# Performance work log

Measured on AMD Instinct MI355X. Metric: run time of the kernel, lower is better.

The kernel has to match this reference:

```python
import jax, jax.numpy as jnp
import numpy as np

TOK, CPC, RHY = 135, 12, 8
HID, STACK, KEY, EMB = 400, 32, 300, 50
B, T = 1, 4096


def setup_inputs() -> dict:
    key = jax.random.key(0)
    ks = jax.random.split(key, 32)
    w = lambda k, shape, s=0.05: jax.random.normal(k, shape, jnp.float32) * s
    inp = {
        'xr': jax.random.randint(ks[0], (B, T), 0, RHY, dtype=jnp.int32),
        'xcpc': jax.random.randint(ks[1], (B, T), 0, CPC, dtype=jnp.int32),
        'xma': jax.random.randint(ks[2], (B, T), 0, TOK, dtype=jnp.int32),
        'emb_midi': w(ks[3], (TOK, EMB)),
        'emb_cpc': w(ks[4], (CPC, EMB)),
        'emb_rhythm': w(ks[5], (RHY, EMB)),
        # note_rnn: 2-layer LSTM, input 3*EMB=150, hidden 400 (torch gate order i,f,g,o)
        'note_Wih0': w(ks[6], (4 * HID, 3 * EMB)),
        'note_Whh0': w(ks[7], (4 * HID, HID)),
        'note_bih0': w(ks[8], (4 * HID,)),
        'note_bhh0': w(ks[9], (4 * HID,)),
        'note_Wih1': w(ks[10], (4 * HID, HID)),
        'note_Whh1': w(ks[11], (4 * HID, HID)),
        'note_bih1': w(ks[12], (4 * HID,)),
        'note_bhh1': w(ks[13], (4 * HID,)),
        'note_fcW': w(ks[14], (3 * EMB, HID)),
        'note_fcb': w(ks[15], (3 * EMB,)),
        # stack memory
        'act_W': w(ks[16], (3, HID)),
        'act_b': w(ks[17], (3,)),
        'D_param': jax.random.normal(ks[18], (1, HID), jnp.float32),
        # key_rnn: 1-layer LSTM, input HID, hidden KEY
        'key_Wih': w(ks[19], (4 * KEY, HID)),
        'key_Whh': w(ks[20], (4 * KEY, KEY)),
        'key_bih': w(ks[21], (4 * KEY,)),
        'key_bhh': w(ks[22], (4 * KEY,)),
        'key_fcW': w(ks[23], (HID, KEY)),
        'key_fcb': w(ks[24], (HID,)),
    }
    return inp


def lstm_layer(x, Wih, Whh, bih, bhh):
    # x: [B,T,I] -> outputs [B,T,H], final (h,c) [B,H]. torch gate order i,f,g,o.
    Bsz = x.shape[0]
    H = Whh.shape[1]
    xg = jnp.einsum('bti,gi->btg', x, Wih) + bih  # precompute input projections

    def step(carry, xt):  # xt: [B,4H]
        h, c = carry
        g = xt + h @ Whh.T + bhh
        i, f, gg, o = jnp.split(g, 4, axis=-1)
        c = jax.nn.sigmoid(f) * c + jax.nn.sigmoid(i) * jnp.tanh(gg)
        h = jax.nn.sigmoid(o) * jnp.tanh(c)
        return (h, c), h

    init = (jnp.zeros((Bsz, H), x.dtype), jnp.zeros((Bsz, H), x.dtype))
    (h, c), hs = jax.lax.scan(step, init, jnp.swapaxes(xg, 0, 1))
    return jnp.swapaxes(hs, 0, 1), h, c


def stack_memory(rnn_out, act_W, act_b, D_param):
    # Per-timestep push/pop/no-op gated stack; returns per-step stack snapshots.
    Bsz, Tlen, H = rnn_out.shape
    probs = jax.nn.softmax(rnn_out @ act_W.T + act_b, axis=-1)            # [B,T,3]
    push_val = jax.nn.sigmoid(jnp.einsum('oh,bth->bt', D_param, rnn_out))  # [B,T]

    def step(s, xs):  # s: [B,STACK,H]
        p, pv = xs  # p: [B,3], pv: [B]
        a = jnp.concatenate([s[:, 1:], s[:, -1:]], axis=1)    # stack[:-1]=stack[1:]
        b = jnp.concatenate([a[:, :1], a[:, :-1]], axis=1)    # stack[1:]=stack[:-1]
        top = p[:, 0:1] * pv[:, None] + p[:, 1:2] * b[:, 1] + p[:, 2:3] * b[:, 0]
        s = b.at[:, 0].set(top)
        return s, s

    init = jnp.zeros((Bsz, STACK, H), rnn_out.dtype)
    _, stacks = jax.lax.scan(step, init, (jnp.swapaxes(probs, 0, 1), push_val.T))
    return jnp.swapaxes(stacks, 0, 1)  # [B,T,STACK,H]


def reference(xr, xcpc, xma, emb_midi, emb_cpc, emb_rhythm,
              note_Wih0, note_Whh0, note_bih0, note_bhh0,
              note_Wih1, note_Whh1, note_bih1, note_bhh1,
              note_fcW, note_fcb, act_W, act_b, D_param,
              key_Wih, key_Whh, key_bih, key_bhh, key_fcW, key_fcb):
    x = jnp.concatenate([emb_midi[xma], emb_cpc[xcpc], emb_rhythm[xr]], axis=2)  # [B,T,150]
    h0, _, _ = lstm_layer(x, note_Wih0, note_Whh0, note_bih0, note_bhh0)
    rnn_out, rh, rc = lstm_layer(h0, note_Wih1, note_Whh1, note_bih1, note_bhh1)
    rtoken_pred = rnn_out @ note_fcW.T + note_fcb  # dropout is identity in eval
    context = stack_memory(rnn_out, act_W, act_b, D_param)  # [B,T,STACK,HID]
    key_in = rh[:, None, :]  # [B,1,HID] (prev_key concat dropped; see notes)
    krnn_out, kh, kc = lstm_layer(key_in, key_Wih, key_Whh, key_bih, key_bhh)
    ktoken_pred = krnn_out @ key_fcW.T + key_fcb  # [B,1,HID]
    return (rtoken_pred, ktoken_pred, context)
```

## Files before the change

kernel.cpp:

```cpp
#include <hip/hip_runtime.h>
#include <stdint.h>

#define T_LEN 4096
#define HID   400
#define G4    1600
#define KDIM  300
#define STACKN 32

__device__ __forceinline__ float fsig(float x){ return 1.f/(1.f + __expf(-x)); }
__device__ __forceinline__ float ftanh(float x){ float e = __expf(2.f*x); return 1.f - 2.f/(e+1.f); }

__global__ void __launch_bounds__(256) kgemm0(
    const int* __restrict__ xma, const int* __restrict__ xcpc, const int* __restrict__ xr,
    const float* __restrict__ em, const float* __restrict__ ec, const float* __restrict__ er,
    const float* __restrict__ W, const float* __restrict__ b1, const float* __restrict__ b2,
    float* __restrict__ XG)
{
  __shared__ float xs[8*152];
  const int t0 = blockIdx.x*8;
  const int tid = threadIdx.x;
  for (int idx = tid; idx < 8*150; idx += 256){
    int tt = idx / 150, k = idx - tt*150;
    int t = t0 + tt;
    float v;
    if (k < 50)       v = em[(size_t)xma[t]*50 + k];
    else if (k < 100) v = ec[(size_t)xcpc[t]*50 + (k-50)];
    else              v = er[(size_t)xr[t]*50 + (k-100)];
    xs[tt*152 + k] = v;
  }
  __syncthreads();
  int r = blockIdx.y*256 + tid;
  if (r >= G4) return;
  float acc[8];
  #pragma unroll
  for (int i=0;i<8;i++) acc[i]=0.f;
  const float2* wr = (const float2*)(W + (size_t)r*150);
  for (int k2=0;k2<75;k2++){
    float2 w = wr[k2];
    int k = 2*k2;
    #pragma unroll
    for (int tt=0;tt<8;tt++)
      acc[tt] += w.x*xs[tt*152+k] + w.y*xs[tt*152+k+1];
  }
  float bb = b1[r] + b2[r];
  #pragma unroll
  for (int tt=0;tt<8;tt++)
    XG[(size_t)(t0+tt)*G4 + r] = acc[tt] + bb;
}

__global__ void __launch_bounds__(512,1) kpipe(
    const float* __restrict__ XG0,
    const float* __restrict__ Whh0, const float* __restrict__ Whh1,
    const float* __restrict__ Wih1, const float* __restrict__ bih1,
    const float* __restrict__ bhh1,
    float* __restrict__ RN,
    unsigned long long* hbufA, unsigned long long* hbufB,
    unsigned long long* gbuf, int T)
{
  const int wid = blockIdx.x;
  const int tid = threadIdx.x;
  const int row_local = tid >> 2;
  const int part = tid & 3;
  const bool mat = (row_local < 100);

  __shared__ float lds_h[HID];
  __shared__ float lds_g[100];
  __shared__ float lds_xg[100];
  __shared__ float lds_hnew[25];

  if (wid < 16){
    const int w = wid;
    float wreg[100];
    if (mat){
      int gate = row_local/25, jj = row_local%25;
      int row = gate*400 + w*25 + jj;
      const float4* wr = (const float4*)(Whh0 + (size_t)row*HID) + part*25;
      #pragma unroll
      for (int i=0;i<25;i++){
        float4 v = wr[i];
        wreg[4*i]=v.x; wreg[4*i+1]=v.y; wreg[4*i+2]=v.z; wreg[4*i+3]=v.w;
      }
    }
    const bool ew = (tid < 25);
    const int j = w*25 + tid;
    float c = 0.f;
    for (int t=0; t<T; t++){
      float xgi=0.f, xgf=0.f, xgg=0.f, xgo=0.f;
      if (ew){
        const float* xrw = XG0 + (size_t)t*G4;
        xgi = xrw[j]; xgf = xrw[HID+j]; xgg = xrw[2*HID+j]; xgo = xrw[3*HID+j];
      }
      if (tid < HID){
        float hv = 0.f;
        if (t > 0){
          if (tid >= w*25 && tid < w*25+25){
            hv = lds_hnew[tid - w*25];
          } else {
            const unsigned long long* src = hbufA + (size_t)(t&3)*HID + tid;
            unsigned long long ex;
            do { ex = __hip_atomic_load(src, __ATOMIC_RELAXED, __HIP_MEMORY_SCOPE_AGENT); }
            while ((unsigned)(ex >> 32) != (unsigned)t);
            union{unsigned u; float f;} cv; cv.u = (unsigned)ex; hv = cv.f;
          }
        }
        lds_h[tid] = hv;
      }
      __syncthreads();
      float sum = 0.f;
      if (mat){
        const float4* hp = (const float4*)(lds_h + part*100);
        #pragma unroll
        for (int i=0;i<25;i++){
          float4 h4 = hp[i];
          sum += wreg[4*i]*h4.x + wreg[4*i+1]*h4.y + wreg[4*i+2]*h4.z + wreg[4*i+3]*h4.w;
        }
      }
      sum += __shfl_xor(sum, 1);
      sum += __shfl_xor(sum, 2);
      if (mat && part==0) lds_g[row_local] = sum;
      __syncthreads();
      if (ew){
        float gi = xgi + lds_g[tid];
        float gf = xgf + lds_g[25+tid];
        float gg = xgg + lds_g[50+tid];
        float go = xgo + lds_g[75+tid];
        float si = fsig(gi), sf = fsig(gf), so = fsig(go), tg = ftanh(gg);
        c = sf*c + si*tg;
        float h = so*ftanh(c);
        lds_hnew[tid] = h;
        union{unsigned u; float f;} cv; cv.f = h;
        unsigned long long pk = ((unsigned long long)(unsigned)(t+1) << 32) | (unsigned long long)cv.u;
        __hip_atomic_store(hbufA + (size_t)((t+1)&3)*HID + j, pk,
                           __ATOMIC_RELAXED, __HIP_MEMORY_SCOPE_AGENT);
      }
      __syncthreads();
    }
  } else if (wid < 32){
    const int f = wid - 16;
    float wreg[100];
    float bias = 0.f;
    int grow = 0;
    if (mat){
      int gate = row_local/25, jj = row_local%25;
      grow = gate*400 + f*25 + jj;
      const float4* wr = (const float4*)(Wih1 + (size_t)grow*HID) + part*25;
      #pragma unroll
      for (int i=0;i<25;i++){
        float4 v = wr[i];
        wreg[4*i]=v.x; wreg[4*i+1]=v.y; wreg[4*i+2]=v.z; wreg[4*i+3]=v.w;
      }
      if (part==0) bias = bih1[grow] + bhh1[grow];
    }
    for (int t=0; t<T; t++){
      if (tid < HID){
        const unsigned long long* src = hbufA + (size_t)((t+1)&3)*HID + tid;
        unsigned long long ex;
        do { ex = __hip_atomic_load(src, __ATOMIC_RELAXED, __HIP_MEMORY_SCOPE_AGENT); }
        while ((unsigned)(ex >> 32) != (unsigned)(t+1));
        union{unsigned u; float f;} cv; cv.u = (unsigned)ex;
        lds_h[tid] = cv.f;
      }
      __syncthreads();
      float sum = 0.f;
      if (mat){
        const float4* hp = (const float4*)(lds_h + part*100);
        #pragma unroll
        for (int i=0;i<25;i++){
          float4 h4 = hp[i];
          sum += wreg[4*i]*h4.x + wreg[4*i+1]*h4.y + wreg[4*i+2]*h4.z + wreg[4*i+3]*h4.w;
        }
      }
      sum += __shfl_xor(sum, 1);
      sum += __shfl_xor(sum, 2);
      if (mat && part==0){
        union{unsigned u; float f;} cv; cv.f = sum + bias;
        unsigned long long pk = ((unsigned long long)(unsigned)(t+1) << 32) | (unsigned long long)cv.u;
        __hip_atomic_store(gbuf + (size_t)((t+1)&3)*G4 + grow, pk,
                           __ATOMIC_RELAXED, __HIP_MEMORY_SCOPE_AGENT);
      }
      __syncthreads();
    }
  } else {
    const int l = wid - 32;
    float wreg[100];
    if (mat){
      int gate = row_local/25, jj = row_local%25;
      int row = gate*400 + l*25 + jj;
      const float4* wr = (const float4*)(Whh1 + (size_t)row*HID) + part*25;
      #pragma unroll
      for (int i=0;i<25;i++){
        float4 v = wr[i];
        wreg[4*i]=v.x; wreg[4*i+1]=v.y; wreg[4*i+2]=v.z; wreg[4*i+3]=v.w;
      }
    }
    const bool ew = (tid < 25);
    const int j = l*25 + tid;
    float c = 0.f;
    for (int t=0; t<T; t++){
      if (tid < HID){
        float hv = 0.f;
        if (t > 0){
          if (tid >= l*25 && tid < l*25+25){
            hv = lds_hnew[tid - l*25];
          } else {
            const unsigned long long* src = hbufB + (size_t)(t&3)*HID + tid;
            unsigned long long ex;
            do { ex = __hip_atomic_load(src, __ATOMIC_RELAXED, __HIP_MEMORY_SCOPE_AGENT); }
            while ((unsigned)(ex >> 32) != (unsigned)t);
            union{unsigned u; float f;} cv; cv.u = (unsigned)ex; hv = cv.f;
          }
        }
        lds_h[tid] = hv;
      } else if (tid < 500){
        int i = tid - 400;
        int gate = i/25, jj = i - gate*25;
        const unsigned long long* src = gbuf + (size_t)((t+1)&3)*G4 + gate*400 + l*25 + jj;
        unsigned long long ex;
        do { ex = __hip_atomic_load(src, __ATOMIC_RELAXED, __HIP_MEMORY_SCOPE_AGENT); }
        while ((unsigned)(ex >> 32) != (unsigned)(t+1));
        union{unsigned u; float f;} cv; cv.u = (unsigned)ex;
        lds_xg[i] = cv.f;
      }
      __syncthreads();
      float sum = 0.f;
      if (mat){
        const float4* hp = (const float4*)(lds_h + part*100);
        #pragma unroll
        for (int i=0;i<25;i++){
          float4 h4 = hp[i];
          sum += wreg[4*i]*h4.x + wreg[4*i+1]*h4.y + wreg[4*i+2]*h4.z + wreg[4*i+3]*h4.w;
        }
      }
      sum += __shfl_xor(sum, 1);
      sum += __shfl_xor(sum, 2);
      if (mat && part==0) lds_g[row_local] = sum;
      __syncthreads();
      if (ew){
        float gi = lds_xg[tid]    + lds_g[tid];
        float gf = lds_xg[25+tid] + lds_g[25+tid];
        float gg = lds_xg[50+tid] + lds_g[50+tid];
        float go = lds_xg[75+tid] + lds_g[75+tid];
        float si = fsig(gi), sf = fsig(gf), so = fsig(go), tg = ftanh(gg);
        c = sf*c + si*tg;
        float h = so*ftanh(c);
        lds_hnew[tid] = h;
        RN[(size_t)t*HID + j] = h;
        union{unsigned u; float f;} cv; cv.f = h;
        unsigned long long pk = ((unsigned long long)(unsigned)(t+1) << 32) | (unsigned long long)cv.u;
        __hip_atomic_store(hbufB + (size_t)((t+1)&3)*HID + j, pk,
                           __ATOMIC_RELAXED, __HIP_MEMORY_SCOPE_AGENT);
      }
      __syncthreads();
    }
  }
}

__global__ void __launch_bounds__(256) krtoken(
    const float* __restrict__ RN, const float* __restrict__ fcW,
    const float* __restrict__ fcb, float* __restrict__ out)
{
  __shared__ float xs[8*400];
  const int t0 = blockIdx.x*8;
  const int tid = threadIdx.x;
  for (int idx = tid; idx < 8*400; idx += 256)
    xs[idx] = RN[(size_t)t0*400 + idx];
  __syncthreads();
  if (tid >= 150) return;
  float acc[8];
  #pragma unroll
  for (int i=0;i<8;i++) acc[i]=0.f;
  const float4* wr = (const float4*)(fcW + (size_t)tid*400);
  for (int k4=0;k4<100;k4++){
    float4 w = wr[k4];
    #pragma unroll
    for (int tt=0;tt<8;tt++){
      const float4 x4 = *(const float4*)(xs + tt*400 + 4*k4);
      acc[tt] += w.x*x4.x + w.y*x4.y + w.z*x4.z + w.w*x4.w;
    }
  }
  float bb = fcb[tid];
  #pragma unroll
  for (int tt=0;tt<8;tt++)
    out[(size_t)(t0+tt)*150 + tid] = acc[tt] + bb;
}

__global__ void kfinal(const float* __restrict__ RN, const float* __restrict__ actW,
                       const float* __restrict__ actb, const float* __restrict__ Dp,
                       float* __restrict__ vbuf)
{
  int t = blockIdx.x, l = threadIdx.x;
  const float* r = RN + (size_t)t*HID;
  float s0=0.f, s1=0.f, s2=0.f, sd=0.f;
  for (int k=l; k<HID; k+=64){
    float rv = r[k];
    s0 += actW[k]*rv;
    s1 += actW[400+k]*rv;
    s2 += actW[800+k]*rv;
    sd += Dp[k]*rv;
  }
  #pragma unroll
  for (int o=1;o<64;o<<=1){
    s0 += __shfl_xor(s0,o); s1 += __shfl_xor(s1,o);
    s2 += __shfl_xor(s2,o); sd += __shfl_xor(sd,o);
  }
  if (l==0){
    s0 += actb[0]; s1 += actb[1]; s2 += actb[2];
    float m = fmaxf(s0, fmaxf(s1, s2));
    float e0 = __expf(s0-m), e1 = __expf(s1-m), e2 = __expf(s2-m);
    float p0 = e0/(e0+e1+e2);
    vbuf[t] = p0 * fsig(sd);
  }
}

__global__ void kctx(const float* __restrict__ vbuf, uint4* __restrict__ ctx, int n16){
  int i = blockIdx.x*256 + threadIdx.x;
  int stride = gridDim.x*256;
  for (; i<n16; i+=stride){
    int t = i / 3200;
    int p = i - t*3200;
    uint4 z;
    if (p < 100){
      float v = vbuf[t];
      union{float f; uint32_t u;} cv; cv.f = v;
      z.x = z.y = z.z = z.w = cv.u;
    } else {
      z.x = z.y = z.z = z.w = 0u;
    }
    ctx[i] = z;
  }
}

__global__ void __launch_bounds__(512) kkey(
    const float* __restrict__ RN, const float* __restrict__ Wih,
    const float* __restrict__ bih, const float* __restrict__ bhh,
    const float* __restrict__ fcW, const float* __restrict__ fcb,
    float* __restrict__ out)
{
  __shared__ float rh[HID];
  __shared__ float gk[4*KDIM];
  __shared__ float hk[KDIM];
  int tid = threadIdx.x;
  if (tid < HID) rh[tid] = RN[(size_t)(T_LEN-1)*HID + tid];
  __syncthreads();
  for (int r = tid; r < 4*KDIM; r += 512){
    const float4* wr = (const float4*)(Wih + (size_t)r*HID);
    float acc = 0.f;
    for (int k4=0;k4<100;k4++){
      float4 w = wr[k4];
      const float4 x4 = *(const float4*)(rh + 4*k4);
      acc += w.x*x4.x + w.y*x4.y + w.z*x4.z + w.w*x4.w;
    }
    gk[r] = acc + bih[r] + bhh[r];
  }
  __syncthreads();
  if (tid < KDIM){
    float gi = gk[tid], gg = gk[2*KDIM+tid], go = gk[3*KDIM+tid];
    float cc = fsig(gi)*ftanh(gg);
    hk[tid] = fsig(go)*ftanh(cc);
  }
  __syncthreads();
  if (tid < HID){
    const float4* wr = (const float4*)(fcW + (size_t)tid*KDIM);
    float acc = 0.f;
    for (int k4=0;k4<75;k4++){
      float4 w = wr[k4];
      const float4 x4 = *(const float4*)(hk + 4*k4);
      acc += w.x*x4.x + w.y*x4.y + w.z*x4.z + w.w*x4.w;
    }
    out[tid] = acc + fcb[tid];
  }
}

extern "C" void kernel_launch(void* const* d_in, const int* in_sizes, int n_in,
                              void* d_out, int out_size, void* d_ws, size_t ws_size,
                              hipStream_t stream)
{
  (void)in_sizes; (void)n_in; (void)ws_size;
  const int*   xr   = (const int*)d_in[0];
  const int*   xcpc = (const int*)d_in[1];
  const int*   xma  = (const int*)d_in[2];
  const float* em   = (const float*)d_in[3];
  const float* ec   = (const float*)d_in[4];
  const float* er   = (const float*)d_in[5];
  const float* Wih0 = (const float*)d_in[6];
  const float* Whh0 = (const float*)d_in[7];
  const float* bih0 = (const float*)d_in[8];
  const float* bhh0 = (const float*)d_in[9];
  const float* Wih1 = (const float*)d_in[10];
  const float* Whh1 = (const float*)d_in[11];
  const float* bih1 = (const float*)d_in[12];
  const float* bhh1 = (const float*)d_in[13];
  const float* fcW  = (const float*)d_in[14];
  const float* fcb  = (const float*)d_in[15];
  const float* actW = (const float*)d_in[16];
  const float* actb = (const float*)d_in[17];
  const float* Dp   = (const float*)d_in[18];
  const float* kWih = (const float*)d_in[19];
  const float* kbih = (const float*)d_in[21];
  const float* kbhh = (const float*)d_in[22];
  const float* kfcW = (const float*)d_in[23];
  const float* kfcb = (const float*)d_in[24];

  float* vbuf = (float*)d_ws;

  float* out = (float*)d_out;
  char*  ob  = (char*)d_out;
  size_t total = (size_t)out_size * 4;
  float* XG0 = (float*)(ob + total - 26214400);
  float* RN  = (float*)(ob + total - 32768000);
  char*  ctl = ob + total - 32768000 - 131072;
  unsigned long long* hbufA = (unsigned long long*)(ctl);
  unsigned long long* hbufB = (unsigned long long*)(ctl + 12800);
  unsigned long long* gbuf  = (unsigned long long*)(ctl + 25600);

  float* rtok = out;
  float* ktok = out + 614400;
  uint4* ctxp = (uint4*)(ob + 614800u*4u);
  int n16 = (int)((total - 614800u*4u) >> 4);

  dim3 gg(T_LEN/8, 7);
  kgemm0<<<gg,256,0,stream>>>(xma, xcpc, xr, em, ec, er, Wih0, bih0, bhh0, XG0);
  kpipe<<<48,512,0,stream>>>(XG0, Whh0, Whh1, Wih1, bih1, bhh1, RN,
                             hbufA, hbufB, gbuf, T_LEN);
  krtoken<<<T_LEN/8,256,0,stream>>>(RN, fcW, fcb, rtok);
  kkey<<<1,512,0,stream>>>(RN, kWih, kbih, kbhh, kfcW, kfcb, ktok);
  kfinal<<<T_LEN,64,0,stream>>>(RN, actW, actb, Dp, vbuf);
  kctx<<<2048,256,0,stream>>>(vbuf, ctxp, n16);
}
```

Measured before the change: 8.501 ms.

## Restructure LSTM pipeline sync: 8-slot ring, pipelined polling, XCD-spread roles, fewer barriers

The persistent LSTM pipeline kernel now launches 128 blocks and keeps only the ones whose blockIdx&7 is 0–2. This presumably spreads the three roles across XCDs. The handoff ring buffers grow from 4 to 8 slots, and polling loads are issued four deep so that spin latency overlaps. The elementwise threads move to a separate wave and read gate inputs directly from global memory instead of staging them through LDS. The trailing barrier per step is removed and replaced by a back-pressure check on layer-1 progress, and the local-h shortcut is dropped. The aim is to cut per-step synchronisation latency on the serial recurrence, at the cost of wasted blocks, more memory polling traffic and subtle ordering risks.

Measured after the change: 10.15 ms. 1.19x slower.

```diff
diff --git a/kernel.cpp b/kernel.cpp
--- a/kernel.cpp
+++ b/kernel.cpp
@@ -9,6 +9,22 @@
 
 __device__ __forceinline__ float fsig(float x){ return 1.f/(1.f + __expf(-x)); }
 __device__ __forceinline__ float ftanh(float x){ float e = __expf(2.f*x); return 1.f - 2.f/(e+1.f); }
+
+__device__ __forceinline__ unsigned long long poll_u64(const unsigned long long* src, unsigned tag){
+  unsigned long long x0 = __hip_atomic_load(src, __ATOMIC_RELAXED, __HIP_MEMORY_SCOPE_AGENT);
+  unsigned long long x1 = __hip_atomic_load(src, __ATOMIC_RELAXED, __HIP_MEMORY_SCOPE_AGENT);
+  unsigned long long x2 = __hip_atomic_load(src, __ATOMIC_RELAXED, __HIP_MEMORY_SCOPE_AGENT);
+  unsigned long long x3 = __hip_atomic_load(src, __ATOMIC_RELAXED, __HIP_MEMORY_SCOPE_AGENT);
+  while ((unsigned)(x0 >> 32) != tag){
+    x0 = x1; x1 = x2; x2 = x3;
+    x3 = __hip_atomic_load(src, __ATOMIC_RELAXED, __HIP_MEMORY_SCOPE_AGENT);
+  }
+  return x0;
+}
+__device__ __forceinline__ float poll_val(const unsigned long long* src, unsigned tag){
+  union{unsigned u; float f;} cv; cv.u = (unsigned)poll_u64(src, tag);
+  return cv.f;
+}
 
 __global__ void __launch_bounds__(256) kgemm0(
     const int* __restrict__ xma, const int* __restrict__ xcpc, const int* __restrict__ xr,
@@ -57,19 +73,21 @@
     unsigned long long* hbufA, unsigned long long* hbufB,
     unsigned long long* gbuf, int T)
 {
-  const int wid = blockIdx.x;
+  const int role = blockIdx.x & 7;
+  if (role > 2) return;
+  const int sub = blockIdx.x >> 3;
   const int tid = threadIdx.x;
   const int row_local = tid >> 2;
   const int part = tid & 3;
-  const bool mat = (row_local < 100);
+  const bool mat = (tid < 400);
+  const bool ew  = (tid >= 448 && tid < 473);
+  const int  ej  = tid - 448;
 
   __shared__ float lds_h[HID];
   __shared__ float lds_g[100];
-  __shared__ float lds_xg[100];
-  __shared__ float lds_hnew[25];
-
-  if (wid < 16){
-    const int w = wid;
+
+  if (role == 0){
+    const int w = sub;
     float wreg[100];
     if (mat){
       int gate = row_local/25, jj = row_local%25;
@@ -81,28 +99,26 @@
         wreg[4*i]=v.x; wreg[4*i+1]=v.y; wreg[4*i+2]=v.z; wreg[4*i+3]=v.w;
       }
     }
-    const bool ew = (tid < 25);
-    const int j = w*25 + tid;
+    const int j = w*25 + ej;
     float c = 0.f;
     for (int t=0; t<T; t++){
       float xgi=0.f, xgf=0.f, xgg=0.f, xgo=0.f;
+      unsigned long long th0=0, th1=0, th2=0, th3=0;
+      const unsigned long long* thp = 0;
       if (ew){
         const float* xrw = XG0 + (size_t)t*G4;
         xgi = xrw[j]; xgf = xrw[HID+j]; xgg = xrw[2*HID+j]; xgo = xrw[3*HID+j];
-      }
-      if (tid < HID){
+        if (t >= 7){
+          thp = hbufB + (size_t)((t-6)&7)*HID + j;
+          th0 = __hip_atomic_load(thp, __ATOMIC_RELAXED, __HIP_MEMORY_SCOPE_AGENT);
+          th1 = __hip_atomic_load(thp, __ATOMIC_RELAXED, __HIP_MEMORY_SCOPE_AGENT);
+          th2 = __hip_atomic_load(thp, __ATOMIC_RELAXED, __HIP_MEMORY_SCOPE_AGENT);
+          th3 = __hip_atomic_load(thp, __ATOMIC_RELAXED, __HIP_MEMORY_SCOPE_AGENT);
+        }
+      }
+      if (mat){
         float hv = 0.f;
-        if (t > 0){
-          if (tid >= w*25 && tid < w*25+25){
-            hv = lds_hnew[tid - w*25];
-          } else {
-            const unsigned long long* src = hbufA + (size_t)(t&3)*HID + tid;
-            unsigned long long ex;
-            do { ex = __hip_atomic_load(src, __ATOMIC_RELAXED, __HIP_MEMORY_SCOPE_AGENT); }
-            while ((unsigned)(ex >> 32) != (unsigned)t);
-            union{unsigned u; float f;} cv; cv.u = (unsigned)ex; hv = cv.f;
-          }
-        }
+        if (t > 0) hv = poll_val(hbufA + (size_t)(t&7)*HID + tid, (unsigned)t);
         lds_h[tid] = hv;
       }
       __syncthreads();
@@ -120,23 +136,28 @@
       if (mat && part==0) lds_g[row_local] = sum;
       __syncthreads();
       if (ew){
-        float gi = xgi + lds_g[tid];
-        float gf = xgf + lds_g[25+tid];
-        float gg = xgg + lds_g[50+tid];
-        float go = xgo + lds_g[75+tid];
+        float gi = xgi + lds_g[ej];
+        float gf = xgf + lds_g[25+ej];
+        float gg = xgg + lds_g[50+ej];
+        float go = xgo + lds_g[75+ej];
         float si = fsig(gi), sf = fsig(gf), so = fsig(go), tg = ftanh(gg);
         c = sf*c + si*tg;
         float h = so*ftanh(c);
-        lds_hnew[tid] = h;
+        if (t >= 7){
+          unsigned want = (unsigned)(t-6);
+          while ((unsigned)(th0 >> 32) != want){
+            th0 = th1; th1 = th2; th2 = th3;
+            th3 = __hip_atomic_load(thp, __ATOMIC_RELAXED, __HIP_MEMORY_SCOPE_AGENT);
+          }
+        }
         union{unsigned u; float f;} cv; cv.f = h;
         unsigned long long pk = ((unsigned long long)(unsigned)(t+1) << 32) | (unsigned long long)cv.u;
-        __hip_atomic_store(hbufA + (size_t)((t+1)&3)*HID + j, pk,
+        __hip_atomic_store(hbufA + (size_t)((t+1)&7)*HID + j, pk,
                            __ATOMIC_RELAXED, __HIP_MEMORY_SCOPE_AGENT);
       }
-      __syncthreads();
-    }
-  } else if (wid < 32){
-    const int f = wid - 16;
+    }
+  } else if (role == 1){
+    const int f = sub;
     float wreg[100];
     float bias = 0.f;
     int grow = 0;
@@ -152,14 +173,8 @@
       if (part==0) bias = bih1[grow] + bhh1[grow];
     }
     for (int t=0; t<T; t++){
-      if (tid < HID){
-        const unsigned long long* src = hbufA + (size_t)((t+1)&3)*HID + tid;
-        unsigned long long ex;
-        do { ex = __hip_atomic_load(src, __ATOMIC_RELAXED, __HIP_MEMORY_SCOPE_AGENT); }
-        while ((unsigned)(ex >> 32) != (unsigned)(t+1));
-        union{unsigned u; float f;} cv; cv.u = (unsigned)ex;
-        lds_h[tid] = cv.f;
-      }
+      if (mat)
+        lds_h[tid] = poll_val(hbufA + (size_t)((t+1)&7)*HID + tid, (unsigned)(t+1));
       __syncthreads();
       float sum = 0.f;
       if (mat){
@@ -175,13 +190,13 @@
       if (mat && part==0){
         union{unsigned u; float f;} cv; cv.f = sum + bias;
         unsigned long long pk = ((unsigned long long)(unsigned)(t+1) << 32) | (unsigned long long)cv.u;
-        __hip_atomic_store(gbuf + (size_t)((t+1)&3)*G4 + grow, pk,
+        __hip_atomic_store(gbuf + (size_t)((t+1)&7)*G4 + grow, pk,
                            __ATOMIC_RELAXED, __HIP_MEMORY_SCOPE_AGENT);
       }
       __syncthreads();
     }
   } else {
-    const int l = wid - 32;
+    const int l = sub;
     float wreg[100];
     if (mat){
       int gate = row_local/25, jj = row_local%25;
@@ -193,35 +208,32 @@
         wreg[4*i]=v.x; wreg[4*i+1]=v.y; wreg[4*i+2]=v.z; wreg[4*i+3]=v.w;
       }
     }
-    const bool ew = (tid < 25);
-    const int j = l*25 + tid;
+    const int j = l*25 + ej;
     float c = 0.f;
     for (int t=0; t<T; t++){
-      if (tid < HID){
+      if (mat){
         float hv = 0.f;
-        if (t > 0){
-          if (tid >= l*25 && tid < l*25+25){
-            hv = lds_hnew[tid - l*25];
-          } else {
-            const unsigned long long* src = hbufB + (size_t)(t&3)*HID + tid;
-            unsigned long long ex;
-            do { ex = __hip_atomic_load(src, __ATOMIC_RELAXED, __HIP_MEMORY_SCOPE_AGENT); }
-            while ((unsigned)(ex >> 32) != (unsigned)t);
-            union{unsigned u; float f;} cv; cv.u = (unsigned)ex; hv = cv.f;
-          }
-        }
+        if (t > 0) hv = poll_val(hbufB + (size_t)(t&7)*HID + tid, (unsigned)t);
         lds_h[tid] = hv;
-      } else if (tid < 500){
-        int i = tid - 400;
-        int gate = i/25, jj = i - gate*25;
-        const unsigned long long* src = gbuf + (size_t)((t+1)&3)*G4 + gate*400 + l*25 + jj;
-        unsigned long long ex;
-        do { ex = __hip_atomic_load(src, __ATOMIC_RELAXED, __HIP_MEMORY_SCOPE_AGENT); }
-        while ((unsigned)(ex >> 32) != (unsigned)(t+1));
-        union{unsigned u; float f;} cv; cv.u = (unsigned)ex;
-        lds_xg[i] = cv.f;
-      }
-      __syncthreads();
+      }
+      __syncthreads();
+      float xg0=0.f, xg1v=0.f, xg2=0.f, xg3=0.f;
+      if (ew){
+        const unsigned long long* gb = gbuf + (size_t)((t+1)&7)*G4 + j;
+        unsigned want = (unsigned)(t+1);
+        unsigned long long v0, v1, v2, v3;
+        for (;;){
+          v0 = __hip_atomic_load(gb,        __ATOMIC_RELAXED, __HIP_MEMORY_SCOPE_AGENT);
+          v1 = __hip_atomic_load(gb + 400,  __ATOMIC_RELAXED, __HIP_MEMORY_SCOPE_AGENT);
+          v2 = __hip_atomic_load(gb + 800,  __ATOMIC_RELAXED, __HIP_MEMORY_SCOPE_AGENT);
+          v3 = __hip_atomic_load(gb + 1200, __ATOMIC_RELAXED, __HIP_MEMORY_SCOPE_AGENT);
+          if (((unsigned)(v0>>32)==want) & ((unsigned)(v1>>32)==want) &
+              ((unsigned)(v2>>32)==want) & ((unsigned)(v3>>32)==want)) break;
+        }
+        union{unsigned u; float f;} c0,c1,c2,c3;
+        c0.u=(unsigned)v0; c1.u=(unsigned)v1; c2.u=(unsigned)v2; c3.u=(unsigned)v3;
+        xg0=c0.f; xg1v=c1.f; xg2=c2.f; xg3=c3.f;
+      }
       float sum = 0.f;
       if (mat){
         const float4* hp = (const float4*)(lds_h + part*100);
@@ -236,21 +248,19 @@
       if (mat && part==0) lds_g[row_local] = sum;
       __syncthreads();
       if (ew){
-        float gi = lds_xg[tid]    + lds_g[tid];
-        float gf = lds_xg[25+tid] + lds_g[25+tid];
-        float gg = lds_xg[50+tid] + lds_g[50+tid];
-        float go = lds_xg[75+tid] + lds_g[75+tid];
+        float gi = xg0  + lds_g[ej];
+        float gf = xg1v + lds_g[25+ej];
+        float gg = xg2  + lds_g[50+ej];
+        float go = xg3  + lds_g[75+ej];
         float si = fsig(gi), sf = fsig(gf), so = fsig(go), tg = ftanh(gg);
         c = sf*c + si*tg;
         float h = so*ftanh(c);
-        lds_hnew[tid] = h;
-        RN[(size_t)t*HID + j] = h;
         union{unsigned u; float f;} cv; cv.f = h;
         unsigned long long pk = ((unsigned long long)(unsigned)(t+1) << 32) | (unsigned long long)cv.u;
-        __hip_atomic_store(hbufB + (size_t)((t+1)&3)*HID + j, pk,
+        __hip_atomic_store(hbufB + (size_t)((t+1)&7)*HID + j, pk,
                            __ATOMIC_RELAXED, __HIP_MEMORY_SCOPE_AGENT);
-      }
-      __syncthreads();
+        RN[(size_t)t*HID + j] = h;
+      }
     }
   }
 }
@@ -408,10 +418,10 @@
   size_t total = (size_t)out_size * 4;
   float* XG0 = (float*)(ob + total - 26214400);
   float* RN  = (float*)(ob + total - 32768000);
-  char*  ctl = ob + total - 32768000 - 131072;
+  char*  ctl = ob + total - 32768000 - 262144;
   unsigned long long* hbufA = (unsigned long long*)(ctl);
-  unsigned long long* hbufB = (unsigned long long*)(ctl + 12800);
-  unsigned long long* gbuf  = (unsigned long long*)(ctl + 25600);
+  unsigned long long* hbufB = (unsigned long long*)(ctl + 25600);
+  unsigned long long* gbuf  = (unsigned long long*)(ctl + 51200);
 
   float* rtok = out;
   float* ktok = out + 614400;
@@ -420,8 +430,8 @@
 
   dim3 gg(T_LEN/8, 7);
   kgemm0<<<gg,256,0,stream>>>(xma, xcpc, xr, em, ec, er, Wih0, bih0, bhh0, XG0);
-  kpipe<<<48,512,0,stream>>>(XG0, Whh0, Whh1, Wih1, bih1, bhh1, RN,
-                             hbufA, hbufB, gbuf, T_LEN);
+  kpipe<<<128,512,0,stream>>>(XG0, Whh0, Whh1, Wih1, bih1, bhh1, RN,
+                              hbufA, hbufB, gbuf, T_LEN);
   krtoken<<<T_LEN/8,256,0,stream>>>(RN, fcW, fcb, rtok);
   kkey<<<1,512,0,stream>>>(RN, kWih, kbih, kbhh, kfcW, kfcb, ktok);
   kfinal<<<T_LEN,64,0,stream>>>(RN, actW, actb, Dp, vbuf);
```

## Pin LSTM pipeline blocks to one XCC and fuse layer-1 input projection

Applied to the files above, without the earlier changes.

Launches many blocks and uses an atomic ticket to keep only 32 blocks that landed on the same XCC as the first, so cross-block handoffs stay within one L2. The layer-1 input projection (Wih1) is fused into the layer-1 recurrent blocks, which removes the separate projection stage and its gbuf handoff. Handoffs are written twice: a workgroup-scope fast copy polled with fetch_add, plus an agent-scope fallback. The ring grows to 32 slots, with occasional back-pressure polls from layer 0 on layer 1. The cost is more registers per block (two weight sets), an extra zeroing kernel, reliance on XCC placement, and polling that may not be coherent at workgroup scope.

Result: slower. 20.68 ms (+143.3%).

```diff
diff --git a/kernel.cpp b/kernel.cpp
--- a/kernel.cpp
+++ b/kernel.cpp
@@ -5,10 +5,39 @@
 #define HID   400
 #define G4    1600
 #define KDIM  300
-#define STACKN 32
+#define RING  32
 
 __device__ __forceinline__ float fsig(float x){ return 1.f/(1.f + __expf(-x)); }
 __device__ __forceinline__ float ftanh(float x){ float e = __expf(2.f*x); return 1.f - 2.f/(e+1.f); }
+
+__device__ __forceinline__ unsigned long long l2_probe(unsigned long long* p){
+  return __hip_atomic_fetch_add(p, 0ull, __ATOMIC_RELAXED, __HIP_MEMORY_SCOPE_WORKGROUP);
+}
+__device__ __forceinline__ void publish_dual(unsigned long long* fast, unsigned long long* safe,
+                                             unsigned tag, float v){
+  union{unsigned u; float f;} c; c.f = v;
+  unsigned long long pk = ((unsigned long long)tag << 32) | (unsigned long long)c.u;
+  *(volatile unsigned long long*)fast = pk;
+  __hip_atomic_store(safe, pk, __ATOMIC_RELAXED, __HIP_MEMORY_SCOPE_AGENT);
+}
+__device__ __forceinline__ float poll_dual(unsigned long long* fast, const unsigned long long* safe,
+                                           unsigned tag){
+  for (int k = 0; k < 24; ++k){
+    unsigned long long x = l2_probe(fast);
+    if ((unsigned)(x >> 32) == tag){
+      union{unsigned u; float f;} c; c.u = (unsigned)x; return c.f;
+    }
+  }
+  unsigned long long x;
+  do { x = __hip_atomic_load(safe, __ATOMIC_RELAXED, __HIP_MEMORY_SCOPE_AGENT); }
+  while ((unsigned)(x >> 32) != tag);
+  union{unsigned u; float f;} c; c.u = (unsigned)x; return c.f;
+}
+
+__global__ void kzero(unsigned long long* __restrict__ p, int n){
+  int i = blockIdx.x*256 + threadIdx.x;
+  if (i < n) p[i] = 0ull;
+}
 
 __global__ void __launch_bounds__(256) kgemm0(
     const int* __restrict__ xma, const int* __restrict__ xcpc, const int* __restrict__ xr,
@@ -48,28 +77,52 @@
     XG[(size_t)(t0+tt)*G4 + r] = acc[tt] + bb;
 }
 
-__global__ void __launch_bounds__(512,1) kpipe(
+__global__ void __launch_bounds__(448,1) kpipe(
     const float* __restrict__ XG0,
     const float* __restrict__ Whh0, const float* __restrict__ Whh1,
     const float* __restrict__ Wih1, const float* __restrict__ bih1,
     const float* __restrict__ bhh1,
     float* __restrict__ RN,
+    unsigned long long* fbufA, unsigned long long* fbufB,
     unsigned long long* hbufA, unsigned long long* hbufB,
-    unsigned long long* gbuf, int T)
-{
-  const int wid = blockIdx.x;
+    unsigned* ctlw, int T)
+{
+  __shared__ int s_slot;
+  __shared__ float lds_h0[HID];
+  __shared__ float lds_h1[HID];
+  __shared__ float lds_g[100];
+  __shared__ float lds_gf[100];
+  __shared__ float lds_hnew[25];
+
+  unsigned xcc;
+  asm volatile("s_getreg_b32 %0, hwreg(HW_REG_XCC_ID)" : "=s"(xcc));
+  if (threadIdx.x == 0){
+    int sl = -1;
+    unsigned tk = atomicAdd(ctlw + 0, 1u);
+    if (tk == 0u)
+      __hip_atomic_store(ctlw + 1, (xcc & 0xffu) | 0x100u,
+                         __ATOMIC_RELAXED, __HIP_MEMORY_SCOPE_AGENT);
+    unsigned ld;
+    do { ld = __hip_atomic_load(ctlw + 1, __ATOMIC_RELAXED, __HIP_MEMORY_SCOPE_AGENT); }
+    while (!(ld & 0x100u));
+    if ((ld & 0xffu) == (xcc & 0xffu)){
+      unsigned t2 = atomicAdd(ctlw + 2, 1u);
+      if (t2 < 32u) sl = (int)t2;
+    }
+    s_slot = sl;
+  }
+  __syncthreads();
+  const int slot = s_slot;
+  if (slot < 0) return;
+
   const int tid = threadIdx.x;
   const int row_local = tid >> 2;
   const int part = tid & 3;
-  const bool mat = (row_local < 100);
-
-  __shared__ float lds_h[HID];
-  __shared__ float lds_g[100];
-  __shared__ float lds_xg[100];
-  __shared__ float lds_hnew[25];
-
-  if (wid < 16){
-    const int w = wid;
+  const bool mat = (tid < 400);
+  const bool ew  = (tid < 25);
+
+  if (slot < 16){
+    const int w = slot;
     float wreg[100];
     if (mat){
       int gate = row_local/25, jj = row_local%25;
@@ -81,7 +134,6 @@
         wreg[4*i]=v.x; wreg[4*i+1]=v.y; wreg[4*i+2]=v.z; wreg[4*i+3]=v.w;
       }
     }
-    const bool ew = (tid < 25);
     const int j = w*25 + tid;
     float c = 0.f;
     for (int t=0; t<T; t++){
@@ -90,25 +142,22 @@
         const float* xrw = XG0 + (size_t)t*G4;
         xgi = xrw[j]; xgf = xrw[HID+j]; xgg = xrw[2*HID+j]; xgo = xrw[3*HID+j];
       }
-      if (tid < HID){
+      if (mat){
         float hv = 0.f;
         if (t > 0){
           if (tid >= w*25 && tid < w*25+25){
             hv = lds_hnew[tid - w*25];
           } else {
-            const unsigned long long* src = hbufA + (size_t)(t&3)*HID + tid;
-            unsigned long long ex;
-            do { ex = __hip_atomic_load(src, __ATOMIC_RELAXED, __HIP_MEMORY_SCOPE_AGENT); }
-            while ((unsigned)(ex >> 32) != (unsigned)t);
-            union{unsigned u; float f;} cv; cv.u = (unsigned)ex; hv = cv.f;
+            int off = (t & (RING-1))*HID + tid;
+            hv = poll_dual(fbufA + off, hbufA + off, (unsigned)t);
           }
         }
-        lds_h[tid] = hv;
+        lds_h0[tid] = hv;
       }
       __syncthreads();
       float sum = 0.f;
       if (mat){
-        const float4* hp = (const float4*)(lds_h + part*100);
+        const float4* hp = (const float4*)(lds_h0 + part*100);
         #pragma unroll
         for (int i=0;i<25;i++){
           float4 h4 = hp[i];
@@ -128,127 +177,78 @@
         c = sf*c + si*tg;
         float h = so*ftanh(c);
         lds_hnew[tid] = h;
-        union{unsigned u; float f;} cv; cv.f = h;
-        unsigned long long pk = ((unsigned long long)(unsigned)(t+1) << 32) | (unsigned long long)cv.u;
-        __hip_atomic_store(hbufA + (size_t)((t+1)&3)*HID + j, pk,
-                           __ATOMIC_RELAXED, __HIP_MEMORY_SCOPE_AGENT);
-      }
-      __syncthreads();
-    }
-  } else if (wid < 32){
-    const int f = wid - 16;
-    float wreg[100];
+        if (t >= 32 && (t & 15) == 0 && tid < 16){
+          int off = ((t-16) & (RING-1))*HID + tid*25;
+          (void)poll_dual(fbufB + off, hbufB + off, (unsigned)(t-16));
+        }
+        int off = ((t+1) & (RING-1))*HID + j;
+        publish_dual(fbufA + off, hbufA + off, (unsigned)(t+1), h);
+      }
+      __syncthreads();
+    }
+  } else {
+    const int l = slot - 16;
+    float wf[100], wh[100];
     float bias = 0.f;
-    int grow = 0;
     if (mat){
       int gate = row_local/25, jj = row_local%25;
-      grow = gate*400 + f*25 + jj;
-      const float4* wr = (const float4*)(Wih1 + (size_t)grow*HID) + part*25;
+      int grow = gate*400 + l*25 + jj;
+      const float4* wr1 = (const float4*)(Wih1 + (size_t)grow*HID) + part*25;
+      const float4* wr2 = (const float4*)(Whh1 + (size_t)grow*HID) + part*25;
       #pragma unroll
       for (int i=0;i<25;i++){
-        float4 v = wr[i];
-        wreg[4*i]=v.x; wreg[4*i+1]=v.y; wreg[4*i+2]=v.z; wreg[4*i+3]=v.w;
+        float4 a = wr1[i]; wf[4*i]=a.x; wf[4*i+1]=a.y; wf[4*i+2]=a.z; wf[4*i+3]=a.w;
+        float4 b = wr2[i]; wh[4*i]=b.x; wh[4*i+1]=b.y; wh[4*i+2]=b.z; wh[4*i+3]=b.w;
       }
       if (part==0) bias = bih1[grow] + bhh1[grow];
     }
-    for (int t=0; t<T; t++){
-      if (tid < HID){
-        const unsigned long long* src = hbufA + (size_t)((t+1)&3)*HID + tid;
-        unsigned long long ex;
-        do { ex = __hip_atomic_load(src, __ATOMIC_RELAXED, __HIP_MEMORY_SCOPE_AGENT); }
-        while ((unsigned)(ex >> 32) != (unsigned)(t+1));
-        union{unsigned u; float f;} cv; cv.u = (unsigned)ex;
-        lds_h[tid] = cv.f;
-      }
-      __syncthreads();
-      float sum = 0.f;
-      if (mat){
-        const float4* hp = (const float4*)(lds_h + part*100);
-        #pragma unroll
-        for (int i=0;i<25;i++){
-          float4 h4 = hp[i];
-          sum += wreg[4*i]*h4.x + wreg[4*i+1]*h4.y + wreg[4*i+2]*h4.z + wreg[4*i+3]*h4.w;
-        }
-      }
-      sum += __shfl_xor(sum, 1);
-      sum += __shfl_xor(sum, 2);
-      if (mat && part==0){
-        union{unsigned u; float f;} cv; cv.f = sum + bias;
-        unsigned long long pk = ((unsigned long long)(unsigned)(t+1) << 32) | (unsigned long long)cv.u;
-        __hip_atomic_store(gbuf + (size_t)((t+1)&3)*G4 + grow, pk,
-                           __ATOMIC_RELAXED, __HIP_MEMORY_SCOPE_AGENT);
-      }
-      __syncthreads();
-    }
-  } else {
-    const int l = wid - 32;
-    float wreg[100];
-    if (mat){
-      int gate = row_local/25, jj = row_local%25;
-      int row = gate*400 + l*25 + jj;
-      const float4* wr = (const float4*)(Whh1 + (size_t)row*HID) + part*25;
-      #pragma unroll
-      for (int i=0;i<25;i++){
-        float4 v = wr[i];
-        wreg[4*i]=v.x; wreg[4*i+1]=v.y; wreg[4*i+2]=v.z; wreg[4*i+3]=v.w;
-      }
-    }
-    const bool ew = (tid < 25);
     const int j = l*25 + tid;
     float c = 0.f;
     for (int t=0; t<T; t++){
-      if (tid < HID){
-        float hv = 0.f;
-        if (t > 0){
-          if (tid >= l*25 && tid < l*25+25){
-            hv = lds_hnew[tid - l*25];
-          } else {
-            const unsigned long long* src = hbufB + (size_t)(t&3)*HID + tid;
-            unsigned long long ex;
-            do { ex = __hip_atomic_load(src, __ATOMIC_RELAXED, __HIP_MEMORY_SCOPE_AGENT); }
-            while ((unsigned)(ex >> 32) != (unsigned)t);
-            union{unsigned u; float f;} cv; cv.u = (unsigned)ex; hv = cv.f;
-          }
+      if (mat){
+        float h1v = 0.f;
+        const bool own = (tid >= l*25 && tid < l*25+25);
+        if (t > 0 && !own){
+          int offb = (t & (RING-1))*HID + tid;
+          h1v = poll_dual(fbufB + offb, hbufB + offb, (unsigned)t);
+        } else if (t > 0){
+          h1v = lds_hnew[tid - l*25];
         }
-        lds_h[tid] = hv;
-      } else if (tid < 500){
-        int i = tid - 400;
-        int gate = i/25, jj = i - gate*25;
-        const unsigned long long* src = gbuf + (size_t)((t+1)&3)*G4 + gate*400 + l*25 + jj;
-        unsigned long long ex;
-        do { ex = __hip_atomic_load(src, __ATOMIC_RELAXED, __HIP_MEMORY_SCOPE_AGENT); }
-        while ((unsigned)(ex >> 32) != (unsigned)(t+1));
-        union{unsigned u; float f;} cv; cv.u = (unsigned)ex;
-        lds_xg[i] = cv.f;
-      }
-      __syncthreads();
-      float sum = 0.f;
+        int offa = ((t+1) & (RING-1))*HID + tid;
+        lds_h0[tid] = poll_dual(fbufA + offa, hbufA + offa, (unsigned)(t+1));
+        lds_h1[tid] = h1v;
+      }
+      __syncthreads();
+      float sumf = 0.f, sumh = 0.f;
       if (mat){
-        const float4* hp = (const float4*)(lds_h + part*100);
+        const float4* hp0 = (const float4*)(lds_h0 + part*100);
+        const float4* hp1 = (const float4*)(lds_h1 + part*100);
         #pragma unroll
         for (int i=0;i<25;i++){
-          float4 h4 = hp[i];
-          sum += wreg[4*i]*h4.x + wreg[4*i+1]*h4.y + wreg[4*i+2]*h4.z + wreg[4*i+3]*h4.w;
+          float4 a = hp0[i];
+          sumf += wf[4*i]*a.x + wf[4*i+1]*a.y + wf[4*i+2]*a.z + wf[4*i+3]*a.w;
+          float4 b = hp1[i];
+          sumh += wh[4*i]*b.x + wh[4*i+1]*b.y + wh[4*i+2]*b.z + wh[4*i+3]*b.w;
         }
       }
-      sum += __shfl_xor(sum, 1);
-      sum += __shfl_xor(sum, 2);
-      if (mat && part==0) lds_g[row_local] = sum;
+      sumf += __shfl_xor(sumf, 1);
+      sumf += __shfl_xor(sumf, 2);
+      sumh += __shfl_xor(sumh, 1);
+      sumh += __shfl_xor(sumh, 2);
+      if (mat && part==0){ lds_gf[row_local] = sumf + bias; lds_g[row_local] = sumh; }
       __syncthreads();
       if (ew){
-        float gi = lds_xg[tid]    + lds_g[tid];
-        float gf = lds_xg[25+tid] + lds_g[25+tid];
-        float gg = lds_xg[50+tid] + lds_g[50+tid];
-        float go = lds_xg[75+tid] + lds_g[75+tid];
-        float si = fsig(gi), sf = fsig(gf), so = fsig(go), tg = ftanh(gg);
-        c = sf*c + si*tg;
+        float gi = lds_gf[tid]    + lds_g[tid];
+        float gf = lds_gf[25+tid] + lds_g[25+tid];
+        float gg = lds_gf[50+tid] + lds_g[50+tid];
+        float go = lds_gf[75+tid] + lds_g[75+tid];
+        float si = fsig(gi), sfo = fsig(gf), so = fsig(go), tg = ftanh(gg);
+        c = sfo*c + si*tg;
         float h = so*ftanh(c);
         lds_hnew[tid] = h;
+        int off = ((t+1) & (RING-1))*HID + j;
+        publish_dual(fbufB + off, hbufB + off, (unsigned)(t+1), h);
         RN[(size_t)t*HID + j] = h;
-        union{unsigned u; float f;} cv; cv.f = h;
-        unsigned long long pk = ((unsigned long long)(unsigned)(t+1) << 32) | (unsigned long long)cv.u;
-        __hip_atomic_store(hbufB + (size_t)((t+1)&3)*HID + j, pk,
-                           __ATOMIC_RELAXED, __HIP_MEMORY_SCOPE_AGENT);
       }
       __syncthreads();
     }
@@ -408,10 +408,13 @@
   size_t total = (size_t)out_size * 4;
   float* XG0 = (float*)(ob + total - 26214400);
   float* RN  = (float*)(ob + total - 32768000);
-  char*  ctl = ob + total - 32768000 - 131072;
-  unsigned long long* hbufA = (unsigned long long*)(ctl);
-  unsigned long long* hbufB = (unsigned long long*)(ctl + 12800);
-  unsigned long long* gbuf  = (unsigned long long*)(ctl + 25600);
+  char*  ctl = ob + total - 32768000 - 524288;
+  unsigned*           ctlw  = (unsigned*)(ctl);
+  unsigned long long* fbufA = (unsigned long long*)(ctl + 4096);
+  unsigned long long* fbufB = (unsigned long long*)(ctl + 4096 + 102400);
+  unsigned long long* hbufA = (unsigned long long*)(ctl + 4096 + 2*102400);
+  unsigned long long* hbufB = (unsigned long long*)(ctl + 4096 + 3*102400);
+  int nz = (4096 + 4*102400) / 8;
 
   float* rtok = out;
   float* ktok = out + 614400;
@@ -419,9 +422,10 @@
   int n16 = (int)((total - 614800u*4u) >> 4);
 
   dim3 gg(T_LEN/8, 7);
+  kzero<<<(nz+255)/256,256,0,stream>>>((unsigned long long*)ctl, nz);
   kgemm0<<<gg,256,0,stream>>>(xma, xcpc, xr, em, ec, er, Wih0, bih0, bhh0, XG0);
-  kpipe<<<48,512,0,stream>>>(XG0, Whh0, Whh1, Wih1, bih1, bhh1, RN,
-                             hbufA, hbufB, gbuf, T_LEN);
+  kpipe<<<2048,448,0,stream>>>(XG0, Whh0, Whh1, Wih1, bih1, bhh1, RN,
+                               fbufA, fbufB, hbufA, hbufB, ctlw, T_LEN);
   krtoken<<<T_LEN/8,256,0,stream>>>(RN, fcW, fcb, rtok);
   kkey<<<1,512,0,stream>>>(RN, kWih, kbih, kbhh, kfcW, kfcb, ktok);
   kfinal<<<T_LEN,64,0,stream>>>(RN, actW, actb, Dp, vbuf);
```
